# Performance work log

Measured on AMD Instinct MI355X. Metric: run time of the kernel, lower is better.

## Reference

```python
import jax, jax.numpy as jnp
import numpy as np

B, S, H, NH = 2, 2048, 512, 8
DK = H // NH


def setup_inputs() -> dict:
    key = jax.random.key(0)
    ks = jax.random.split(key, 12)
    inp = {
        "query": jax.random.normal(ks[0], (B, S, H), dtype=jnp.float32),
        "key": jax.random.normal(ks[1], (B, S, H), dtype=jnp.float32),
        "value": jax.random.normal(ks[2], (B, S, H), dtype=jnp.float32),
        "bias": jax.random.normal(ks[3], (B, 1, S, S), dtype=jnp.float32),
        "mask": jax.random.randint(ks[4], (B, S), 0, 2, dtype=jnp.int32),
        "Wq": jax.random.normal(ks[5], (H, H), dtype=jnp.float32) * 0.02,
        "bq": jax.random.normal(ks[6], (H,), dtype=jnp.float32) * 0.02,
        "Wk": jax.random.normal(ks[7], (H, H), dtype=jnp.float32) * 0.02,
        "bk": jax.random.normal(ks[8], (H,), dtype=jnp.float32) * 0.02,
        "Wv": jax.random.normal(ks[9], (H, H), dtype=jnp.float32) * 0.02,
        "bv": jax.random.normal(ks[10], (H,), dtype=jnp.float32) * 0.02,
    }
    return inp


def reference(query, key, value, bias, mask, Wq, bq, Wk, bk, Wv, bv):
    b = query.shape[0]
    # torch nn.Linear: x @ W.T + b, then split heads -> [B, h, S, d_k]
    def proj(x, W, bb):
        y = x @ W.T + bb
        return y.reshape(b, -1, NH, DK).transpose(0, 2, 1, 3)

    q = proj(query, Wq, bq)
    k = proj(key, Wk, bk)
    v = proj(value, Wv, bv)

    score = jnp.einsum("bhqd,bhkd->bhqk", q, k) / np.sqrt(DK).astype(np.float32)
    # NOTE: the source swaps bias/mask when calling attention():
    #   the 0/1 mask is ADDED to the scores...
    mask_add = mask.reshape(b, 1, 1, -1).astype(score.dtype)
    score = score + mask_add
    #   ...and the float bias is used for the masked_fill (bias == 0 -> -1e30).
    score = jnp.where(bias == 0, jnp.asarray(-1e30, score.dtype), score)
    attn = jax.nn.softmax(score, axis=-1)  # dropout=None in the source call
    x = jnp.einsum("bhqk,bhkd->bhqd", attn, v)
    return x.transpose(0, 2, 1, 3).reshape(b, -1, NH * DK)
```

## Files before the change

### kernel.cpp

```cpp
#include <hip/hip_runtime.h>
#include <hip/hip_bf16.h>
#include <stdint.h>

#define B_  2
#define S_  2048
#define H_  512
#define NH_ 8
#define DK_ 64

typedef __bf16 bf16x8 __attribute__((ext_vector_type(8)));
typedef short  s16x4  __attribute__((ext_vector_type(4)));
typedef float  f32x4  __attribute__((ext_vector_type(4)));

static __device__ __forceinline__ uint32_t pk2(float a, float b) {
  __hip_bfloat162 h = __float22bfloat162_rn(float2{a, b});
  uint32_t u;
  __builtin_memcpy(&u, &h, 4);
  return u;
}

static __device__ __forceinline__ f32x4 mfma_k16(s16x4 a, s16x4 b, f32x4 c) {
#if defined(__HIP_DEVICE_COMPILE__)
  return __builtin_amdgcn_mfma_f32_16x16x16bf16_1k(a, b, c, 0, 0, 0);
#else
  (void)a; (void)b;
  return c;
#endif
}

typedef const __attribute__((address_space(1))) uint32_t* gas_t;
typedef __attribute__((address_space(3))) uint32_t* las_t;
static __device__ __forceinline__ void cp16(const void* g, void* l) {
  __builtin_amdgcn_global_load_lds((gas_t)g, (las_t)l, 16, 0, 0);
}

struct ProjArgs {
  const float* X[3];
  const float* W[3];
  const float* Bv[3];
  uint16_t*    O[3];
  const float* bias;
  const int*   mask;
  uint32_t*    zrow;
  float*       fmL;
};

__global__ __launch_bounds__(256) void prep_proj_kernel(ProjArgs pa) {
  __shared__ __align__(16) char psm[16512];
  int bid = blockIdx.x, t = threadIdx.x;

  if (bid >= 1536) {
    if (bid < 2048) {
      int rr = bid - 1536;
      const float* base = pa.bias + (size_t)rr * 8 * 2048 + t * 8;
      uint4 a[8], b2[8];
#pragma unroll
      for (int i = 0; i < 8; i++) {
        const uint4* src = (const uint4*)(base + (size_t)i * 2048);
        a[i] = src[0]; b2[i] = src[1];
      }
      uint32_t (*wbuf)[4] = (uint32_t (*)[4])psm;
      int wv = t >> 6, ln = t & 63;
#pragma unroll
      for (int i = 0; i < 8; i++) {
        bool z = ((a[i].x << 1) == 0u) | ((a[i].y << 1) == 0u) |
                 ((a[i].z << 1) == 0u) | ((a[i].w << 1) == 0u) |
                 ((b2[i].x << 1) == 0u) | ((b2[i].y << 1) == 0u) |
                 ((b2[i].z << 1) == 0u) | ((b2[i].w << 1) == 0u);
        uint64_t m = __ballot(z);
        if (ln == 0) {
          uint32_t bits = 0;
#pragma unroll
          for (int c = 0; c < 8; c++)
            bits |= (uint32_t)(((m >> (8 * c)) & 0xFFull) != 0ull) << c;
          wbuf[i][wv] = bits;
        }
      }
      __syncthreads();
      if (t < 8)
        pa.zrow[rr * 8 + t] = wbuf[t][0] | (wbuf[t][1] << 8) |
                              (wbuf[t][2] << 16) | (wbuf[t][3] << 24);
    } else {
      const float LOG2E = 1.44269504088896340736f;
#pragma unroll
      for (int i = 0; i < 16; i++) {
        int idx = i * 256 + t;
        pa.fmL[idx] = (float)pa.mask[idx] * LOG2E;
      }
    }
    return;
  }

  int xcd = bid & 7, j = bid >> 3;
  int gi = ((j >> 3) << 3) | xcd;
  int dtile = j & 7;
  int mat = gi >> 6, mtile = gi & 63;
  int m0 = mtile * 64, n0 = dtile * 64;
  const float* X  = pa.X[mat];
  const float* Wt = pa.W[mat];
  const float* Bv = pa.Bv[mat];
  uint16_t*    O  = pa.O[mat];

  uint16_t (*Xs)[64] = (uint16_t (*)[64])psm;
  uint16_t (*Ws)[64] = (uint16_t (*)[64])(psm + 8192);

  int w = t >> 6, l = t & 63, lo = l & 15, g = l >> 4;
  int tr = t >> 4;
  int lc = t & 15;

  const float* Xp = X + (size_t)(m0 + tr) * 512 + lc * 4;
  const float* Wp = Wt + (size_t)(n0 + tr) * 512 + lc * 4;

  f32x4 acc[4];
#pragma unroll
  for (int dt = 0; dt < 4; dt++) acc[dt] = (f32x4){0.f, 0.f, 0.f, 0.f};

  float4 xa[4], wa2[4];
#pragma unroll
  for (int i = 0; i < 4; i++) {
    xa[i]  = *(const float4*)(Xp + (size_t)i * 16 * 512);
    wa2[i] = *(const float4*)(Wp + (size_t)i * 16 * 512);
  }

  for (int kb = 0; kb < 8; kb++) {
#pragma unroll
    for (int i = 0; i < 4; i++) {
      int r = i * 16 + tr;
      int s0 = (lc >> 1) ^ (r & 7);
      uint2 pkx{pk2(xa[i].x, xa[i].y), pk2(xa[i].z, xa[i].w)};
      *(uint2*)&Xs[r][s0 * 8 + (lc & 1) * 4] = pkx;
      uint2 pkw{pk2(wa2[i].x, wa2[i].y), pk2(wa2[i].z, wa2[i].w)};
      *(uint2*)&Ws[r][s0 * 8 + (lc & 1) * 4] = pkw;
    }
    __syncthreads();
    if (kb < 7) {
      const float* Xn = Xp + (kb + 1) * 64;
      const float* Wn = Wp + (kb + 1) * 64;
#pragma unroll
      for (int i = 0; i < 4; i++) {
        xa[i]  = *(const float4*)(Xn + (size_t)i * 16 * 512);
        wa2[i] = *(const float4*)(Wn + (size_t)i * 16 * 512);
      }
    }
#pragma unroll
    for (int kk = 0; kk < 2; kk++) {
      int seg = (kk * 4 + g) ^ (lo & 7);
      bf16x8 xf = *(const bf16x8*)&Xs[w * 16 + lo][seg * 8];
      bf16x8 wf[4];
#pragma unroll
      for (int dt = 0; dt < 4; dt++)
        wf[dt] = *(const bf16x8*)&Ws[dt * 16 + lo][seg * 8];
      if (mat < 2) {
#pragma unroll
        for (int dt = 0; dt < 4; dt++)
          acc[dt] = __builtin_amdgcn_mfma_f32_16x16x32_bf16(wf[dt], xf, acc[dt], 0, 0, 0);
      } else {
#pragma unroll
        for (int dt = 0; dt < 4; dt++)
          acc[dt] = __builtin_amdgcn_mfma_f32_16x16x32_bf16(xf, wf[dt], acc[dt], 0, 0, 0);
      }
    }
    __syncthreads();
  }

  if (mat < 2) {
    float scale = (mat == 0) ? 0.125f : 1.0f;
    float4 bv4[4];
#pragma unroll
    for (int dt = 0; dt < 4; dt++)
      bv4[dt] = *(const float4*)(Bv + n0 + dt * 16 + g * 4);
    int ss = m0 + w * 16 + lo;
    int bb = ss >> 11, sIn = ss & 2047;
    uint16_t* obase = O + ((size_t)(bb * NH_ + dtile) * S_ + sIn) * DK_;
#pragma unroll
    for (int dt = 0; dt < 4; dt++) {
      float v0 = (acc[dt][0] + bv4[dt].x) * scale;
      float v1 = (acc[dt][1] + bv4[dt].y) * scale;
      float v2 = (acc[dt][2] + bv4[dt].z) * scale;
      float v3 = (acc[dt][3] + bv4[dt].w) * scale;
      uint2 pk{pk2(v0, v1), pk2(v2, v3)};
      *(uint2*)(obase + dt * 16 + g * 4) = pk;
    }
  } else {
    float bval[4];
#pragma unroll
    for (int dt = 0; dt < 4; dt++) bval[dt] = Bv[n0 + dt * 16 + lo];
    int m = m0 + w * 16 + g * 4;
    int bb = m >> 11, sIn = m & 2047;
#pragma unroll
    for (int dt = 0; dt < 4; dt++) {
      int dd = dt * 16 + lo;
      float v0 = acc[dt][0] + bval[dt];
      float v1 = acc[dt][1] + bval[dt];
      float v2 = acc[dt][2] + bval[dt];
      float v3 = acc[dt][3] + bval[dt];
      uint2 pk{pk2(v0, v1), pk2(v2, v3)};
      *(uint2*)(O + ((size_t)(bb * NH_ + dtile) * DK_ + dd) * S_ + sIn) = pk;
    }
  }
}

__global__ __launch_bounds__(256, 2) void attn_kernel(
    const uint16_t* __restrict__ Qb, const uint16_t* __restrict__ Kb,
    const uint16_t* __restrict__ Vt, const uint32_t* __restrict__ zrow,
    const float* __restrict__ fmL, const float* __restrict__ bias,
    float* __restrict__ out) {
  int bid = blockIdx.x;
  int bh = bid & 15, qtile = bid >> 4;
  int b = bh >> 3, h = bh & 7;
  int q0 = qtile * 32;
  int t = threadIdx.x;
  int w = t >> 6, l = t & 63, lo = l & 15, g = l >> 4;

  __shared__ __align__(16) char smem[32768];
  uint16_t* KsB = (uint16_t*)smem;
  uint16_t* VsB = (uint16_t*)(smem + 16384);

  const uint16_t* Qh = Qb + (size_t)bh * S_ * DK_;
  const uint16_t* Kh = Kb + (size_t)bh * S_ * DK_;
  const uint16_t* Vh = Vt + (size_t)bh * DK_ * S_;

  int lrow = l >> 3, lseg = (l & 7) ^ lrow;
  const uint16_t* kbase = Kh + (size_t)(w * 16 + lrow) * DK_ + lseg * 8;
  const uint16_t* vbase = Vh + (size_t)(w * 16 + lrow) * S_ + lseg * 8;
  uint16_t* kd0 = KsB + (w * 16) * 64;
  uint16_t* kd8 = KsB + (w * 16 + 8) * 64;
  uint16_t* vd0 = VsB + (w * 16) * 64;
  uint16_t* vd8 = VsB + (w * 16 + 8) * 64;

  uint32_t zall = zrow[(b << 11) + q0 + (l & 31)];
#pragma unroll
  for (int s = 1; s < 32; s <<= 1) zall |= __shfl_xor(zall, s);

  bf16x8 qf[2][2];
#pragma unroll
  for (int qt = 0; qt < 2; qt++)
#pragma unroll
    for (int kk = 0; kk < 2; kk++)
      qf[qt][kk] = *(const bf16x8*)(Qh + (size_t)(q0 + qt * 16 + lo) * DK_ + kk * 32 + g * 8);

  f32x4 o[4][2];
#pragma unroll
  for (int dt = 0; dt < 4; dt++)
#pragma unroll
    for (int qt = 0; qt < 2; qt++) o[dt][qt] = (f32x4){0.f, 0.f, 0.f, 0.f};
  float ts[2] = {0.f, 0.f};

  const float* fmrow = fmL + b * S_ + w * 16 + g * 4;
  const float LOG2E = 1.44269504088896340736f;

  cp16(kbase, kd0);
  cp16(kbase + 512, kd8);
  cp16(vbase, vd0);
  cp16(vbase + 8 * S_, vd8);

  for (int kb = 0; kb < 32; kb++) {
    int cur = kb & 1;
    int k0 = kb * 64;
    float4 mv4 = *(const float4*)(fmrow + k0);
    __syncthreads();
    if (kb + 1 < 32) {
      int kn = k0 + 64;
      int nb = (cur ^ 1) * 4096;
      cp16(kbase + (size_t)kn * 64, kd0 + nb);
      cp16(kbase + (size_t)kn * 64 + 512, kd8 + nb);
      cp16(vbase + kn, vd0 + nb);
      cp16(vbase + kn + 8 * S_, vd8 + nb);
    }
    const uint16_t* KsT = KsB + cur * 4096;
    const uint16_t* VsT = VsB + cur * 4096;

    s16x4 vf[4];
    {
      int s = (2 * w + (g >> 1)) ^ (lo & 7);
      int off = s * 8 + (g & 1) * 4;
#pragma unroll
      for (int dt = 0; dt < 4; dt++)
        vf[dt] = *(const s16x4*)(VsT + (dt * 16 + lo) * 64 + off);
    }
    bf16x8 kf[2];
#pragma unroll
    for (int kk = 0; kk < 2; kk++) {
      int s = (kk * 4 + g) ^ (lo & 7);
      kf[kk] = *(const bf16x8*)(KsT + (w * 16 + lo) * 64 + s * 8);
    }

    f32x4 c[2];
#pragma unroll
    for (int qt = 0; qt < 2; qt++) {
      f32x4 z = {0.f, 0.f, 0.f, 0.f};
      z = __builtin_amdgcn_mfma_f32_16x16x32_bf16(kf[0], qf[qt][0], z, 0, 0, 0);
      c[qt] = __builtin_amdgcn_mfma_f32_16x16x32_bf16(kf[1], qf[qt][1], z, 0, 0, 0);
    }

    float p[2][4];
    if (((zall >> kb) & 1u) == 0u) {
#pragma unroll
      for (int qt = 0; qt < 2; qt++) {
        p[qt][0] = __builtin_amdgcn_exp2f(__builtin_fmaf(c[qt][0], LOG2E, mv4.x));
        p[qt][1] = __builtin_amdgcn_exp2f(__builtin_fmaf(c[qt][1], LOG2E, mv4.y));
        p[qt][2] = __builtin_amdgcn_exp2f(__builtin_fmaf(c[qt][2], LOG2E, mv4.z));
        p[qt][3] = __builtin_amdgcn_exp2f(__builtin_fmaf(c[qt][3], LOG2E, mv4.w));
      }
    } else {
#pragma unroll
      for (int qt = 0; qt < 2; qt++) {
        float4 bz = *(const float4*)(bias + ((size_t)(b * S_ + q0 + qt * 16 + lo)) * S_ + k0 + w * 16 + g * 4);
        p[qt][0] = (bz.x == 0.f) ? 0.f : __builtin_amdgcn_exp2f(__builtin_fmaf(c[qt][0], LOG2E, mv4.x));
        p[qt][1] = (bz.y == 0.f) ? 0.f : __builtin_amdgcn_exp2f(__builtin_fmaf(c[qt][1], LOG2E, mv4.y));
        p[qt][2] = (bz.z == 0.f) ? 0.f : __builtin_amdgcn_exp2f(__builtin_fmaf(c[qt][2], LOG2E, mv4.z));
        p[qt][3] = (bz.w == 0.f) ? 0.f : __builtin_amdgcn_exp2f(__builtin_fmaf(c[qt][3], LOG2E, mv4.w));
      }
    }

    s16x4 pf[2];
#pragma unroll
    for (int qt = 0; qt < 2; qt++) {
      ts[qt] += (p[qt][0] + p[qt][1]) + (p[qt][2] + p[qt][3]);
      union { s16x4 v; uint32_t u[2]; } uu;
      uu.u[0] = pk2(p[qt][0], p[qt][1]);
      uu.u[1] = pk2(p[qt][2], p[qt][3]);
      pf[qt] = uu.v;
    }

#pragma unroll
    for (int dt = 0; dt < 4; dt++)
#pragma unroll
      for (int qt = 0; qt < 2; qt++)
        o[dt][qt] = mfma_k16(vf[dt], pf[qt], o[dt][qt]);
  }

  float* OT = (float*)smem;
  float* LS = (float*)(smem + 8448);
#pragma unroll
  for (int qt = 0; qt < 2; qt++) {
    float v = ts[qt];
    v += __shfl_xor(v, 16);
    v += __shfl_xor(v, 32);
    ts[qt] = v;
  }
  __syncthreads();
  if (g == 0) {
#pragma unroll
    for (int qt = 0; qt < 2; qt++) LS[(w * 2 + qt) * 16 + lo] = ts[qt];
  }
#pragma unroll
  for (int ww = 0; ww < 4; ww++) {
    if (w == ww) {
#pragma unroll
      for (int dt = 0; dt < 4; dt++)
#pragma unroll
        for (int qt = 0; qt < 2; qt++)
#pragma unroll
          for (int r = 0; r < 4; r++) {
            int idx = (dt * 16 + g * 4 + r) * 33 + qt * 16 + lo;
            if (ww == 0) OT[idx] = o[dt][qt][r];
            else         OT[idx] += o[dt][qt][r];
          }
    }
    __syncthreads();
  }
  {
    int q = t >> 3, dseg = (t & 7) * 8;
    int qt2 = q >> 4, lo2 = q & 15;
    float lsum = LS[(0 * 2 + qt2) * 16 + lo2] + LS[(1 * 2 + qt2) * 16 + lo2] +
                 LS[(2 * 2 + qt2) * 16 + lo2] + LS[(3 * 2 + qt2) * 16 + lo2];
    float linv = 1.0f / fmaxf(lsum, 1e-30f);
    float* ob = out + ((size_t)(b * S_ + q0 + q)) * H_ + h * DK_ + dseg;
#pragma unroll
    for (int i = 0; i < 2; i++) {
      float4 v;
      v.x = OT[(dseg + i * 4 + 0) * 33 + q] * linv;
      v.y = OT[(dseg + i * 4 + 1) * 33 + q] * linv;
      v.z = OT[(dseg + i * 4 + 2) * 33 + q] * linv;
      v.w = OT[(dseg + i * 4 + 3) * 33 + q] * linv;
      *(float4*)(ob + i * 4) = v;
    }
  }
}

extern "C" void kernel_launch(void* const* d_in, const int* in_sizes, int n_in,
                              void* d_out, int out_size, void* d_ws, size_t ws_size,
                              hipStream_t stream) {
  const float* query = (const float*)d_in[0];
  const float* key   = (const float*)d_in[1];
  const float* value = (const float*)d_in[2];
  const float* bias  = (const float*)d_in[3];
  const int*   mask  = (const int*)d_in[4];
  const float* Wq = (const float*)d_in[5];
  const float* bq = (const float*)d_in[6];
  const float* Wk = (const float*)d_in[7];
  const float* bk = (const float*)d_in[8];
  const float* Wv = (const float*)d_in[9];
  const float* bv = (const float*)d_in[10];

  char* ws = (char*)d_ws;
  uint32_t* zrow = (uint32_t*)ws;
  float*    fmL  = (float*)(ws + 16384);
  uint16_t* Qb = (uint16_t*)(ws + (size_t)(1 << 20));
  uint16_t* Kb = (uint16_t*)(ws + (size_t)(5 << 20));
  uint16_t* Vt = (uint16_t*)(ws + (size_t)(9 << 20));

  ProjArgs pa;
  pa.X[0] = query; pa.X[1] = key; pa.X[2] = value;
  pa.W[0] = Wq;    pa.W[1] = Wk;  pa.W[2] = Wv;
  pa.Bv[0] = bq;   pa.Bv[1] = bk; pa.Bv[2] = bv;
  pa.O[0] = Qb;    pa.O[1] = Kb;  pa.O[2] = Vt;
  pa.bias = bias;  pa.mask = mask;
  pa.zrow = zrow;  pa.fmL = fmL;

  prep_proj_kernel<<<2049, 256, 0, stream>>>(pa);

  attn_kernel<<<1024, 256, 0, stream>>>(Qb, Kb, Vt, zrow, fmL, bias, (float*)d_out);
}
```

Baseline: 162.3 us.

## Use 8 waves per attention block with 128-key tiles and split reduction

Doubles the attention block to 512 threads (8 waves), each covering 16 keys of a 128-key tile, which halves the number of loop iterations and barriers per block. The K/V shared-memory tiles are widened to 128 keys with a new XOR swizzle for V, and the per-wave partial outputs are reduced into two shared buffers that are summed in the final store. Shared memory per block doubles to 64 KB, and the launch bounds request 4 blocks per CU, which may constrain registers and limit occupancy.

```diff
diff --git a/kernel.cpp b/kernel.cpp
--- a/kernel.cpp
+++ b/kernel.cpp
@@ -200,7 +200,7 @@
   }
 }
 
-__global__ __launch_bounds__(256, 2) void attn_kernel(
+__global__ __launch_bounds__(512, 4) void attn_kernel(
     const uint16_t* __restrict__ Qb, const uint16_t* __restrict__ Kb,
     const uint16_t* __restrict__ Vt, const uint32_t* __restrict__ zrow,
     const float* __restrict__ fmL, const float* __restrict__ bias,
@@ -212,9 +212,9 @@
   int t = threadIdx.x;
   int w = t >> 6, l = t & 63, lo = l & 15, g = l >> 4;
 
-  __shared__ __align__(16) char smem[32768];
+  __shared__ __align__(16) char smem[65536];
   uint16_t* KsB = (uint16_t*)smem;
-  uint16_t* VsB = (uint16_t*)(smem + 16384);
+  uint16_t* VsB = (uint16_t*)(smem + 32768);
 
   const uint16_t* Qh = Qb + (size_t)bh * S_ * DK_;
   const uint16_t* Kh = Kb + (size_t)bh * S_ * DK_;
@@ -222,11 +222,16 @@
 
   int lrow = l >> 3, lseg = (l & 7) ^ lrow;
   const uint16_t* kbase = Kh + (size_t)(w * 16 + lrow) * DK_ + lseg * 8;
-  const uint16_t* vbase = Vh + (size_t)(w * 16 + lrow) * S_ + lseg * 8;
   uint16_t* kd0 = KsB + (w * 16) * 64;
   uint16_t* kd8 = KsB + (w * 16 + 8) * 64;
-  uint16_t* vd0 = VsB + (w * 16) * 64;
-  uint16_t* vd8 = VsB + (w * 16 + 8) * 64;
+  int vr4 = l >> 4;
+  int vs16 = l & 15;
+  int vrow0 = w * 8 + vr4;
+  int vrow1 = w * 8 + 4 + vr4;
+  const uint16_t* vb0 = Vh + (size_t)vrow0 * S_ + ((vs16 ^ (vrow0 & 15)) * 8);
+  const uint16_t* vb1 = Vh + (size_t)vrow1 * S_ + ((vs16 ^ (vrow1 & 15)) * 8);
+  uint16_t* vd0 = VsB + (w * 8) * 128;
+  uint16_t* vd1 = VsB + (w * 8 + 4) * 128;
 
   uint32_t zall = zrow[(b << 11) + q0 + (l & 31)];
 #pragma unroll
@@ -250,39 +255,40 @@
   const float LOG2E = 1.44269504088896340736f;
 
   cp16(kbase, kd0);
-  cp16(kbase + 512, kd8);
-  cp16(vbase, vd0);
-  cp16(vbase + 8 * S_, vd8);
-
-  for (int kb = 0; kb < 32; kb++) {
+  cp16(kbase + 8 * DK_, kd8);
+  cp16(vb0, vd0);
+  cp16(vb1, vd1);
+
+  for (int kb = 0; kb < 16; kb++) {
     int cur = kb & 1;
-    int k0 = kb * 64;
+    int k0 = kb * 128;
     float4 mv4 = *(const float4*)(fmrow + k0);
     __syncthreads();
-    if (kb + 1 < 32) {
-      int kn = k0 + 64;
-      int nb = (cur ^ 1) * 4096;
-      cp16(kbase + (size_t)kn * 64, kd0 + nb);
-      cp16(kbase + (size_t)kn * 64 + 512, kd8 + nb);
-      cp16(vbase + kn, vd0 + nb);
-      cp16(vbase + kn + 8 * S_, vd8 + nb);
-    }
-    const uint16_t* KsT = KsB + cur * 4096;
-    const uint16_t* VsT = VsB + cur * 4096;
+    if (kb + 1 < 16) {
+      int kn = k0 + 128;
+      int nb = (cur ^ 1) * 8192;
+      cp16(kbase + (size_t)kn * DK_, kd0 + nb);
+      cp16(kbase + (size_t)kn * DK_ + 8 * DK_, kd8 + nb);
+      cp16(vb0 + kn, vd0 + nb);
+      cp16(vb1 + kn, vd1 + nb);
+    }
+    const uint16_t* KsT = KsB + cur * 8192;
+    const uint16_t* VsT = VsB + cur * 8192;
 
     s16x4 vf[4];
     {
-      int s = (2 * w + (g >> 1)) ^ (lo & 7);
-      int off = s * 8 + (g & 1) * 4;
-#pragma unroll
-      for (int dt = 0; dt < 4; dt++)
-        vf[dt] = *(const s16x4*)(VsT + (dt * 16 + lo) * 64 + off);
+      int sl = 2 * w + (g >> 1);
+#pragma unroll
+      for (int dt = 0; dt < 4; dt++) {
+        int sp = sl ^ lo;
+        vf[dt] = *(const s16x4*)(VsT + (dt * 16 + lo) * 128 + sp * 8 + (g & 1) * 4);
+      }
     }
     bf16x8 kf[2];
 #pragma unroll
     for (int kk = 0; kk < 2; kk++) {
-      int s = (kk * 4 + g) ^ (lo & 7);
-      kf[kk] = *(const bf16x8*)(KsT + (w * 16 + lo) * 64 + s * 8);
+      int sp = (kk * 4 + g) ^ (lo & 7);
+      kf[kk] = *(const bf16x8*)(KsT + (w * 16 + lo) * 64 + sp * 8);
     }
 
     f32x4 c[2];
@@ -294,7 +300,7 @@
     }
 
     float p[2][4];
-    if (((zall >> kb) & 1u) == 0u) {
+    if (((zall >> (2 * kb)) & 3u) == 0u) {
 #pragma unroll
       for (int qt = 0; qt < 2; qt++) {
         p[qt][0] = __builtin_amdgcn_exp2f(__builtin_fmaf(c[qt][0], LOG2E, mv4.x));
@@ -330,8 +336,9 @@
         o[dt][qt] = mfma_k16(vf[dt], pf[qt], o[dt][qt]);
   }
 
-  float* OT = (float*)smem;
-  float* LS = (float*)(smem + 8448);
+  float* OTA = (float*)smem;
+  float* OTB = (float*)(smem + 8448);
+  float* LS  = (float*)(smem + 16896);
 #pragma unroll
   for (int qt = 0; qt < 2; qt++) {
     float v = ts[qt];
@@ -344,9 +351,10 @@
 #pragma unroll
     for (int qt = 0; qt < 2; qt++) LS[(w * 2 + qt) * 16 + lo] = ts[qt];
   }
+  float* OT = (w < 4) ? OTA : OTB;
 #pragma unroll
   for (int ww = 0; ww < 4; ww++) {
-    if (w == ww) {
+    if ((w & 3) == ww) {
 #pragma unroll
       for (int dt = 0; dt < 4; dt++)
 #pragma unroll
@@ -361,21 +369,19 @@
     __syncthreads();
   }
   {
-    int q = t >> 3, dseg = (t & 7) * 8;
+    int q = t >> 4, dcol = (t & 15) * 4;
     int qt2 = q >> 4, lo2 = q & 15;
-    float lsum = LS[(0 * 2 + qt2) * 16 + lo2] + LS[(1 * 2 + qt2) * 16 + lo2] +
-                 LS[(2 * 2 + qt2) * 16 + lo2] + LS[(3 * 2 + qt2) * 16 + lo2];
+    float lsum = 0.f;
+#pragma unroll
+    for (int ww = 0; ww < 8; ww++) lsum += LS[(ww * 2 + qt2) * 16 + lo2];
     float linv = 1.0f / fmaxf(lsum, 1e-30f);
-    float* ob = out + ((size_t)(b * S_ + q0 + q)) * H_ + h * DK_ + dseg;
-#pragma unroll
-    for (int i = 0; i < 2; i++) {
-      float4 v;
-      v.x = OT[(dseg + i * 4 + 0) * 33 + q] * linv;
-      v.y = OT[(dseg + i * 4 + 1) * 33 + q] * linv;
-      v.z = OT[(dseg + i * 4 + 2) * 33 + q] * linv;
-      v.w = OT[(dseg + i * 4 + 3) * 33 + q] * linv;
-      *(float4*)(ob + i * 4) = v;
-    }
+    float* ob = out + ((size_t)(b * S_ + q0 + q)) * H_ + h * DK_ + dcol;
+    float4 v;
+    v.x = (OTA[(dcol + 0) * 33 + q] + OTB[(dcol + 0) * 33 + q]) * linv;
+    v.y = (OTA[(dcol + 1) * 33 + q] + OTB[(dcol + 1) * 33 + q]) * linv;
+    v.z = (OTA[(dcol + 2) * 33 + q] + OTB[(dcol + 2) * 33 + q]) * linv;
+    v.w = (OTA[(dcol + 3) * 33 + q] + OTB[(dcol + 3) * 33 + q]) * linv;
+    *(float4*)ob = v;
   }
 }
 
@@ -411,5 +417,5 @@
 
   prep_proj_kernel<<<2049, 256, 0, stream>>>(pa);
 
-  attn_kernel<<<1024, 256, 0, stream>>>(Qb, Kb, Vt, zrow, fmL, bias, (float*)d_out);
-}
+  attn_kernel<<<1024, 512, 0, stream>>>(Qb, Kb, Vt, zrow, fmL, bias, (float*)d_out);
+}
```

After: 169.8 us. 4.6% more time.

## Load K/V fragments directly from global into registers, dropping LDS staging

Applied to the files above, without the earlier changes.

Replaces the double-buffered global-to-LDS async copies of K and V tiles with direct per-lane global loads into registers, prefetched one iteration ahead. This removes the per-iteration __syncthreads and LDS reads, and shrinks shared memory to what the epilogue reduction needs. The trade-off is less coalesced global loads, especially the strided 8-byte V fragment reads, relying on cache hits instead of LDS reuse.

```diff
diff --git a/kernel.cpp b/kernel.cpp
--- a/kernel.cpp
+++ b/kernel.cpp
@@ -26,12 +26,6 @@
   (void)a; (void)b;
   return c;
 #endif
-}
-
-typedef const __attribute__((address_space(1))) uint32_t* gas_t;
-typedef __attribute__((address_space(3))) uint32_t* las_t;
-static __device__ __forceinline__ void cp16(const void* g, void* l) {
-  __builtin_amdgcn_global_load_lds((gas_t)g, (las_t)l, 16, 0, 0);
 }
 
 struct ProjArgs {
@@ -212,22 +206,12 @@
   int t = threadIdx.x;
   int w = t >> 6, l = t & 63, lo = l & 15, g = l >> 4;
 
-  __shared__ __align__(16) char smem[32768];
-  uint16_t* KsB = (uint16_t*)smem;
-  uint16_t* VsB = (uint16_t*)(smem + 16384);
+  __shared__ __align__(16) char smem[8960];
 
   const uint16_t* Qh = Qb + (size_t)bh * S_ * DK_;
   const uint16_t* Kh = Kb + (size_t)bh * S_ * DK_;
   const uint16_t* Vh = Vt + (size_t)bh * DK_ * S_;
 
-  int lrow = l >> 3, lseg = (l & 7) ^ lrow;
-  const uint16_t* kbase = Kh + (size_t)(w * 16 + lrow) * DK_ + lseg * 8;
-  const uint16_t* vbase = Vh + (size_t)(w * 16 + lrow) * S_ + lseg * 8;
-  uint16_t* kd0 = KsB + (w * 16) * 64;
-  uint16_t* kd8 = KsB + (w * 16 + 8) * 64;
-  uint16_t* vd0 = VsB + (w * 16) * 64;
-  uint16_t* vd8 = VsB + (w * 16 + 8) * 64;
-
   uint32_t zall = zrow[(b << 11) + q0 + (l & 31)];
 #pragma unroll
   for (int s = 1; s < 32; s <<= 1) zall |= __shfl_xor(zall, s);
@@ -246,55 +230,48 @@
     for (int qt = 0; qt < 2; qt++) o[dt][qt] = (f32x4){0.f, 0.f, 0.f, 0.f};
   float ts[2] = {0.f, 0.f};
 
-  const float* fmrow = fmL + b * S_ + w * 16 + g * 4;
+  const uint16_t* kpB = Kh + (size_t)(w * 16 + lo) * DK_ + g * 8;
+  const uint16_t* vpB = Vh + (size_t)lo * S_ + w * 16 + g * 4;
+  const float*    fb  = fmL + b * S_ + w * 16 + g * 4;
   const float LOG2E = 1.44269504088896340736f;
 
-  cp16(kbase, kd0);
-  cp16(kbase + 512, kd8);
-  cp16(vbase, vd0);
-  cp16(vbase + 8 * S_, vd8);
-
-  for (int kb = 0; kb < 32; kb++) {
-    int cur = kb & 1;
-    int k0 = kb * 64;
-    float4 mv4 = *(const float4*)(fmrow + k0);
-    __syncthreads();
-    if (kb + 1 < 32) {
-      int kn = k0 + 64;
-      int nb = (cur ^ 1) * 4096;
-      cp16(kbase + (size_t)kn * 64, kd0 + nb);
-      cp16(kbase + (size_t)kn * 64 + 512, kd8 + nb);
-      cp16(vbase + kn, vd0 + nb);
-      cp16(vbase + kn + 8 * S_, vd8 + nb);
-    }
-    const uint16_t* KsT = KsB + cur * 4096;
-    const uint16_t* VsT = VsB + cur * 4096;
-
-    s16x4 vf[4];
-    {
-      int s = (2 * w + (g >> 1)) ^ (lo & 7);
-      int off = s * 8 + (g & 1) * 4;
+  bf16x8 kf2[2][2];
+  s16x4  vf2[2][4];
+  float4 mv2[2];
+  {
+    kf2[0][0] = *(const bf16x8*)(kpB);
+    kf2[0][1] = *(const bf16x8*)(kpB + 32);
+#pragma unroll
+    for (int dt = 0; dt < 4; dt++)
+      vf2[0][dt] = *(const s16x4*)(vpB + (size_t)dt * 16 * S_);
+    mv2[0] = *(const float4*)fb;
+  }
+
+#pragma unroll 2
+  for (int j = 0; j < 32; j++) {
+    int cb = j & 1;
+    if (j + 1 < 32) {
+      const uint16_t* kp = kpB + (size_t)(j + 1) * 64 * DK_;
+      kf2[cb ^ 1][0] = *(const bf16x8*)(kp);
+      kf2[cb ^ 1][1] = *(const bf16x8*)(kp + 32);
+      const uint16_t* vp = vpB + (j + 1) * 64;
 #pragma unroll
       for (int dt = 0; dt < 4; dt++)
-        vf[dt] = *(const s16x4*)(VsT + (dt * 16 + lo) * 64 + off);
-    }
-    bf16x8 kf[2];
-#pragma unroll
-    for (int kk = 0; kk < 2; kk++) {
-      int s = (kk * 4 + g) ^ (lo & 7);
-      kf[kk] = *(const bf16x8*)(KsT + (w * 16 + lo) * 64 + s * 8);
+        vf2[cb ^ 1][dt] = *(const s16x4*)(vp + (size_t)dt * 16 * S_);
+      mv2[cb ^ 1] = *(const float4*)(fb + (j + 1) * 64);
     }
 
     f32x4 c[2];
 #pragma unroll
     for (int qt = 0; qt < 2; qt++) {
       f32x4 z = {0.f, 0.f, 0.f, 0.f};
-      z = __builtin_amdgcn_mfma_f32_16x16x32_bf16(kf[0], qf[qt][0], z, 0, 0, 0);
-      c[qt] = __builtin_amdgcn_mfma_f32_16x16x32_bf16(kf[1], qf[qt][1], z, 0, 0, 0);
-    }
-
+      z = __builtin_amdgcn_mfma_f32_16x16x32_bf16(kf2[cb][0], qf[qt][0], z, 0, 0, 0);
+      c[qt] = __builtin_amdgcn_mfma_f32_16x16x32_bf16(kf2[cb][1], qf[qt][1], z, 0, 0, 0);
+    }
+
+    float4 mv4 = mv2[cb];
     float p[2][4];
-    if (((zall >> kb) & 1u) == 0u) {
+    if (((zall >> j) & 1u) == 0u) {
 #pragma unroll
       for (int qt = 0; qt < 2; qt++) {
         p[qt][0] = __builtin_amdgcn_exp2f(__builtin_fmaf(c[qt][0], LOG2E, mv4.x));
@@ -305,7 +282,7 @@
     } else {
 #pragma unroll
       for (int qt = 0; qt < 2; qt++) {
-        float4 bz = *(const float4*)(bias + ((size_t)(b * S_ + q0 + qt * 16 + lo)) * S_ + k0 + w * 16 + g * 4);
+        float4 bz = *(const float4*)(bias + ((size_t)(b * S_ + q0 + qt * 16 + lo)) * S_ + j * 64 + w * 16 + g * 4);
         p[qt][0] = (bz.x == 0.f) ? 0.f : __builtin_amdgcn_exp2f(__builtin_fmaf(c[qt][0], LOG2E, mv4.x));
         p[qt][1] = (bz.y == 0.f) ? 0.f : __builtin_amdgcn_exp2f(__builtin_fmaf(c[qt][1], LOG2E, mv4.y));
         p[qt][2] = (bz.z == 0.f) ? 0.f : __builtin_amdgcn_exp2f(__builtin_fmaf(c[qt][2], LOG2E, mv4.z));
@@ -327,7 +304,7 @@
     for (int dt = 0; dt < 4; dt++)
 #pragma unroll
       for (int qt = 0; qt < 2; qt++)
-        o[dt][qt] = mfma_k16(vf[dt], pf[qt], o[dt][qt]);
+        o[dt][qt] = mfma_k16(vf2[cb][dt], pf[qt], o[dt][qt]);
   }
 
   float* OT = (float*)smem;
@@ -339,7 +316,6 @@
     v += __shfl_xor(v, 32);
     ts[qt] = v;
   }
-  __syncthreads();
   if (g == 0) {
 #pragma unroll
     for (int qt = 0; qt < 2; qt++) LS[(w * 2 + qt) * 16 + lo] = ts[qt];
```

Result: slower. 218.3 us (+34.5%).

## Make attention K/V tiles wave-private to drop per-iteration block barriers

Applied to the files above, without the earlier changes.

The V tile layout changes so each wave copies and reads only its own 16-key slice, matching K, which is already wave-private. That lets the per-iteration __syncthreads be replaced by an s_waitcnt vmcnt on the async copies. The additive-mask row is staged once into shared memory instead of being read from global memory every iteration, and launch bounds are raised to 4 blocks per SM to allow more occupancy. A wrap-around prefetch keeps the outstanding-load count constant, but it issues one redundant tile load at the end that could race with the epilogue's reuse of shared memory.

```diff
diff --git a/kernel.cpp b/kernel.cpp
--- a/kernel.cpp
+++ b/kernel.cpp
@@ -200,7 +200,7 @@
   }
 }
 
-__global__ __launch_bounds__(256, 2) void attn_kernel(
+__global__ __launch_bounds__(256, 4) void attn_kernel(
     const uint16_t* __restrict__ Qb, const uint16_t* __restrict__ Kb,
     const uint16_t* __restrict__ Vt, const uint32_t* __restrict__ zrow,
     const float* __restrict__ fmL, const float* __restrict__ bias,
@@ -212,9 +212,10 @@
   int t = threadIdx.x;
   int w = t >> 6, l = t & 63, lo = l & 15, g = l >> 4;
 
-  __shared__ __align__(16) char smem[32768];
-  uint16_t* KsB = (uint16_t*)smem;
-  uint16_t* VsB = (uint16_t*)(smem + 16384);
+  __shared__ __align__(16) char smem[40960];
+  uint16_t* Kbuf = (uint16_t*)smem;
+  uint16_t* Vbuf = (uint16_t*)(smem + 16384);
+  float*    fmb  = (float*)(smem + 32768);
 
   const uint16_t* Qh = Qb + (size_t)bh * S_ * DK_;
   const uint16_t* Kh = Kb + (size_t)bh * S_ * DK_;
@@ -222,11 +223,13 @@
 
   int lrow = l >> 3, lseg = (l & 7) ^ lrow;
   const uint16_t* kbase = Kh + (size_t)(w * 16 + lrow) * DK_ + lseg * 8;
-  const uint16_t* vbase = Vh + (size_t)(w * 16 + lrow) * S_ + lseg * 8;
-  uint16_t* kd0 = KsB + (w * 16) * 64;
-  uint16_t* kd8 = KsB + (w * 16 + 8) * 64;
-  uint16_t* vd0 = VsB + (w * 16) * 64;
-  uint16_t* vd8 = VsB + (w * 16 + 8) * 64;
+  uint16_t* kd0 = Kbuf + (w * 16) * 64;
+  uint16_t* kd8 = Kbuf + (w * 16 + 8) * 64;
+  int vdr = l >> 1, vkh = l & 1;
+  const uint16_t* vb0 = Vh + (size_t)vdr * S_ + w * 16 + vkh * 8;
+  const uint16_t* vb1 = Vh + (size_t)(32 + vdr) * S_ + w * 16 + vkh * 8;
+  uint16_t* vdst0 = Vbuf + w * 1024;
+  uint16_t* vdst1 = Vbuf + w * 1024 + 512;
 
   uint32_t zall = zrow[(b << 11) + q0 + (l & 31)];
 #pragma unroll
@@ -246,43 +249,47 @@
     for (int qt = 0; qt < 2; qt++) o[dt][qt] = (f32x4){0.f, 0.f, 0.f, 0.f};
   float ts[2] = {0.f, 0.f};
 
-  const float* fmrow = fmL + b * S_ + w * 16 + g * 4;
   const float LOG2E = 1.44269504088896340736f;
 
   cp16(kbase, kd0);
-  cp16(kbase + 512, kd8);
-  cp16(vbase, vd0);
-  cp16(vbase + 8 * S_, vd8);
-
-  for (int kb = 0; kb < 32; kb++) {
-    int cur = kb & 1;
-    int k0 = kb * 64;
-    float4 mv4 = *(const float4*)(fmrow + k0);
-    __syncthreads();
-    if (kb + 1 < 32) {
-      int kn = k0 + 64;
-      int nb = (cur ^ 1) * 4096;
-      cp16(kbase + (size_t)kn * 64, kd0 + nb);
-      cp16(kbase + (size_t)kn * 64 + 512, kd8 + nb);
-      cp16(vbase + kn, vd0 + nb);
-      cp16(vbase + kn + 8 * S_, vd8 + nb);
-    }
-    const uint16_t* KsT = KsB + cur * 4096;
-    const uint16_t* VsT = VsB + cur * 4096;
+  cp16(kbase + 8 * DK_, kd8);
+  cp16(vb0, vdst0);
+  cp16(vb1, vdst1);
+  {
+    const float4* ms = (const float4*)(fmL + (size_t)b * S_ + t * 8);
+    float4 m0 = ms[0], m1 = ms[1];
+    *(float4*)(fmb + t * 8) = m0;
+    *(float4*)(fmb + t * 8 + 4) = m1;
+  }
+  __syncthreads();
+
+#pragma unroll 2
+  for (int j = 0; j < 32; j++) {
+    int cb = j & 1;
+    {
+      int jn = (j + 1) & 31;
+      int nb = (cb ^ 1) * 4096;
+      cp16(kbase + (size_t)jn * 64 * DK_, kd0 + nb);
+      cp16(kbase + (size_t)jn * 64 * DK_ + 8 * DK_, kd8 + nb);
+      cp16(vb0 + jn * 64, vdst0 + nb);
+      cp16(vb1 + jn * 64, vdst1 + nb);
+    }
+    asm volatile("s_waitcnt vmcnt(4)" ::: "memory");
+
+    const uint16_t* KsT = Kbuf + cb * 4096;
+    const uint16_t* VsT = Vbuf + cb * 4096 + w * 1024;
+
+    float4 mv4 = *(const float4*)(fmb + j * 64 + w * 16 + g * 4);
 
     s16x4 vf[4];
-    {
-      int s = (2 * w + (g >> 1)) ^ (lo & 7);
-      int off = s * 8 + (g & 1) * 4;
-#pragma unroll
-      for (int dt = 0; dt < 4; dt++)
-        vf[dt] = *(const s16x4*)(VsT + (dt * 16 + lo) * 64 + off);
-    }
+#pragma unroll
+    for (int dt = 0; dt < 4; dt++)
+      vf[dt] = *(const s16x4*)(VsT + (dt * 16 + lo) * 16 + g * 4);
     bf16x8 kf[2];
 #pragma unroll
     for (int kk = 0; kk < 2; kk++) {
-      int s = (kk * 4 + g) ^ (lo & 7);
-      kf[kk] = *(const bf16x8*)(KsT + (w * 16 + lo) * 64 + s * 8);
+      int sp = (kk * 4 + g) ^ (lo & 7);
+      kf[kk] = *(const bf16x8*)(KsT + (w * 16 + lo) * 64 + sp * 8);
     }
 
     f32x4 c[2];
@@ -294,7 +301,7 @@
     }
 
     float p[2][4];
-    if (((zall >> kb) & 1u) == 0u) {
+    if (((zall >> j) & 1u) == 0u) {
 #pragma unroll
       for (int qt = 0; qt < 2; qt++) {
         p[qt][0] = __builtin_amdgcn_exp2f(__builtin_fmaf(c[qt][0], LOG2E, mv4.x));
@@ -305,7 +312,7 @@
     } else {
 #pragma unroll
       for (int qt = 0; qt < 2; qt++) {
-        float4 bz = *(const float4*)(bias + ((size_t)(b * S_ + q0 + qt * 16 + lo)) * S_ + k0 + w * 16 + g * 4);
+        float4 bz = *(const float4*)(bias + ((size_t)(b * S_ + q0 + qt * 16 + lo)) * S_ + j * 64 + w * 16 + g * 4);
         p[qt][0] = (bz.x == 0.f) ? 0.f : __builtin_amdgcn_exp2f(__builtin_fmaf(c[qt][0], LOG2E, mv4.x));
         p[qt][1] = (bz.y == 0.f) ? 0.f : __builtin_amdgcn_exp2f(__builtin_fmaf(c[qt][1], LOG2E, mv4.y));
         p[qt][2] = (bz.z == 0.f) ? 0.f : __builtin_amdgcn_exp2f(__builtin_fmaf(c[qt][2], LOG2E, mv4.z));
@@ -330,6 +337,7 @@
         o[dt][qt] = mfma_k16(vf[dt], pf[qt], o[dt][qt]);
   }
 
+  __syncthreads();
   float* OT = (float*)smem;
   float* LS = (float*)(smem + 8448);
 #pragma unroll
@@ -339,7 +347,6 @@
     v += __shfl_xor(v, 32);
     ts[qt] = v;
   }
-  __syncthreads();
   if (g == 0) {
 #pragma unroll
     for (int qt = 0; qt < 2; qt++) LS[(w * 2 + qt) * 16 + lo] = ts[qt];
```

After: 177.2 us. 9.2% more time.
